# Performance work log

Measured on AMD Instinct MI355X. Metric: run time of the kernel, lower is better.

## Reference

```python
import jax, jax.numpy as jnp
import numpy as np

EPS = 1e-5  # torch BatchNorm1d default eps
NUM_CLASSES = 10


def setup_inputs() -> dict:
    key = jax.random.key(0)
    ks = jax.random.split(key, 8)
    N, M, D = 8192, 8192, 256
    h1, h2 = 128, 64
    x = jax.random.normal(ks[0], (N, D), dtype=jnp.float32)
    x_n = jax.random.normal(ks[1], (M, D), dtype=jnp.float32)
    y_n = jax.random.randint(ks[2], (M,), 0, NUM_CLASSES)
    # Linear weights (torch layout [out, in]) and biases
    W0 = jax.random.normal(ks[3], (h1, D), dtype=jnp.float32) * 0.05
    b0 = jnp.zeros((h1,), dtype=jnp.float32)
    W1 = jax.random.normal(ks[4], (h2, h1), dtype=jnp.float32) * 0.05
    b1 = jnp.zeros((h2,), dtype=jnp.float32)
    # BatchNorm1d affine params (torch init: weight=1, bias=0)
    g0 = jnp.ones((h1,), dtype=jnp.float32)
    bt0 = jnp.zeros((h1,), dtype=jnp.float32)
    g1 = jnp.ones((h2,), dtype=jnp.float32)
    bt1 = jnp.zeros((h2,), dtype=jnp.float32)
    return {"x": x, "x_n": x_n, "y_n": y_n,
            "W0": W0, "b0": b0, "g0": g0, "bt0": bt0,
            "W1": W1, "b1": b1, "g1": g1, "bt1": bt1}


def _bn(h, gamma, beta):
    # BatchNorm1d in training mode: batch mean / biased batch var per feature
    m = jnp.mean(h, axis=0)
    v = jnp.var(h, axis=0)
    return gamma * (h - m) / jnp.sqrt(v + EPS) + beta


def _feats(z, params):
    # fcn stack: BatchNorm(Tanh(Linear(z)))
    for W, b, g, bt in params:
        z = _bn(jnp.tanh(z @ W.T + b), g, bt)
    return z


def reference(x, x_n, y_n, W0, b0, g0, bt0, W1, b1, g1, bt1):
    params = [(W0, b0, g0, bt0), (W1, b1, g1, bt1)]
    q = _feats(x, params)    # [N, 64]
    k = _feats(x_n, params)  # [M, 64]
    # euclidean cdist via the quadratic expansion
    d2 = (jnp.sum(q * q, axis=1)[:, None]
          + jnp.sum(k * k, axis=1)[None, :]
          - 2.0 * (q @ k.T))
    sim = jnp.sqrt(jnp.maximum(d2, 1e-12))  # [N, M]
    sim = jnp.max(sim) - sim                 # larger = nearer
    # x != x_n here, so no self-mask branch (matches torch.equal check)
    p = jax.nn.softmax(sim, axis=1)          # [N, M]
    y1h = jax.nn.one_hot(y_n, NUM_CLASSES, dtype=p.dtype)  # [M, C]
    return jnp.clip(p @ y1h, 0.0, 1.0)       # [N, C]
```

## Files before the change

kernel.cpp:

```cpp
#include <hip/hip_runtime.h>
#include <math.h>

#define EPSBN 1e-5f
#define AADD(p, v) __hip_atomic_fetch_add((p), (v), __ATOMIC_RELAXED, __HIP_MEMORY_SCOPE_AGENT)

typedef unsigned short u16;
typedef short bf16x8 __attribute__((ext_vector_type(8)));
typedef float f32x4 __attribute__((ext_vector_type(4)));
typedef float f32x16 __attribute__((ext_vector_type(16)));
typedef int i32x4 __attribute__((ext_vector_type(4)));

constexpr int NROWS = 8192;
constexpr int NCLS = 10;
constexpr int MPAD = 8832;
constexpr int NT_PAD = 138;
constexpr int GY = 6;
constexpr int TPG = 23;
constexpr float SCL  = 2.0813689810056077f;
constexpr float SCL2 = -4.1627379620112154f;

constexpr size_t OFF_W0P = 0;
constexpr size_t OFF_H1H = 32768;
constexpr size_t OFF_H1L = OFF_H1H + 1048576;
constexpr size_t OFF_SUM = OFF_H1L + 1048576;
constexpr size_t OFF_W1P = OFF_SUM + 768;
constexpr size_t OFF_B1E = OFF_W1P + 16384;
constexpr size_t OFF_H2  = OFF_B1E + 128;
constexpr size_t OFF_PIDX = OFF_H2 + 1048576;
constexpr size_t OFF_TCLS = OFF_PIDX + MPAD;
constexpr size_t OFF_QH  = OFF_H1H;
constexpr size_t OFF_QL  = OFF_QH + 262144;
constexpr size_t OFF_QN2 = OFF_QL + 262144;
constexpr size_t OFF_KH  = OFF_QN2 + NROWS;
constexpr size_t OFF_KL  = OFF_KH + 282624;
constexpr size_t OFF_KN2 = OFF_KL + 282624;
constexpr size_t OFF_PART = OFF_H2;

__device__ inline u16 f2bf(float f) {
  unsigned u = __float_as_uint(f);
  unsigned r = (u + 0x7fffu + ((u >> 16) & 1u)) >> 16;
  return (u16)r;
}
__device__ inline float bf2f(u16 h) { return __uint_as_float(((unsigned)h) << 16); }

__device__ inline float tanh_fast(float x) {
  float e = __builtin_amdgcn_exp2f(x * 2.88539008f);
  return 1.f - 2.f * __builtin_amdgcn_rcpf(e + 1.f);
}

__global__ __launch_bounds__(256) void k_prep(
    const float* __restrict__ w0, const int* __restrict__ yn,
    u16* __restrict__ w0p, int* __restrict__ pidx, int* __restrict__ tcls,
    float* __restrict__ sums)
{
  if (blockIdx.x < 128) {
    int idx = blockIdx.x * 256 + threadIdx.x;
    int t = idx & 255;
    float v = w0[idx];
    u16 hi = f2bf(v);
    u16 lo = f2bf(v - bf2f(hi));
    int j = idx >> 8;
    w0p[(t >> 3) * 1024 + j * 8 + (t & 7)] = hi;
    w0p[32768 + (t >> 3) * 1024 + j * 8 + (t & 7)] = lo;
    return;
  }
  __shared__ int cnt[256][NCLS];
  __shared__ int wtot[4][NCLS];
  __shared__ int pstart[NCLS + 1];
  const int t = threadIdx.x;
  const int lane = t & 63, wv = t >> 6;
  sums[t] = 0.f; sums[t + 256] = 0.f; sums[t + 512] = 0.f;
  #pragma unroll
  for (int c = 0; c < NCLS; ++c) cnt[t][c] = 0;
  for (int i = t; i < MPAD; i += 256) pidx[i] = -1;
  for (int i = t; i < NROWS; i += 256) cnt[t][yn[i]]++;
  __syncthreads();
  #pragma unroll
  for (int c = 0; c < NCLS; ++c) {
    int x = cnt[t][c];
    int inc = x;
    #pragma unroll
    for (int d = 1; d < 64; d <<= 1) { int y = __shfl_up(inc, d); if (lane >= d) inc += y; }
    if (lane == 63) wtot[wv][c] = inc;
    cnt[t][c] = inc - x;
  }
  __syncthreads();
  if (t == 0) {
    int run = 0;
    #pragma unroll
    for (int c = 0; c < NCLS; ++c) {
      int tot = wtot[0][c] + wtot[1][c] + wtot[2][c] + wtot[3][c];
      pstart[c] = run;
      int ntile = (tot + 63) >> 6;
      for (int tt = 0; tt < ntile; ++tt) tcls[(run >> 6) + tt] = c;
      run += ntile << 6;
    }
    pstart[NCLS] = run;
    for (int tt = run >> 6; tt < NT_PAD; ++tt) tcls[tt] = NCLS;
  }
  __syncthreads();
  #pragma unroll
  for (int c = 0; c < NCLS; ++c) {
    int add = pstart[c];
    for (int w2 = 0; w2 < 4; ++w2) if (w2 < wv) add += wtot[w2][c];
    cnt[t][c] += add;
  }
  __syncthreads();
  for (int i = t; i < NROWS; i += 256) {
    int c = yn[i];
    pidx[cnt[t][c]++] = i;
  }
}

__global__ __launch_bounds__(256) void k_layer1(
    const float* __restrict__ x, const float* __restrict__ xn,
    const u16* __restrict__ w0p, const float* __restrict__ b0,
    u16* __restrict__ h1h, u16* __restrict__ h1l, float* __restrict__ sums)
{
  const int tid = threadIdx.x;
  const int w = tid >> 6, l = tid & 63;
  const int l15 = l & 15, l4 = l >> 4;
  const int blk = blockIdx.x;
  const int rowHalf = w & 1, colHalf = w >> 1;
  const int r0 = blk * 32 + 16 * rowHalf;
  const int c0 = 64 * colHalf;
  const int b = (blk < 256) ? 0 : 1;
  const float* src = (blk < 256) ? (x + (size_t)blk * 32 * 256)
                                 : (xn + (size_t)(blk - 256) * 32 * 256);
  const float* xrow = src + (size_t)(16 * rowHalf + l15) * 256;

  f32x4 acc[4];
  #pragma unroll
  for (int ct = 0; ct < 4; ++ct) acc[ct] = (f32x4){0.f, 0.f, 0.f, 0.f};

  #pragma unroll
  for (int ks = 0; ks < 8; ++ks) {
    const float* xp = xrow + ks * 32 + l4 * 8;
    f32x4 a0 = *(const f32x4*)xp;
    f32x4 a1 = *(const f32x4*)(xp + 4);
    bf16x8 ah, al_;
    #pragma unroll
    for (int i = 0; i < 4; ++i) {
      u16 h = f2bf(a0[i]); ah[i] = (short)h; al_[i] = (short)f2bf(a0[i] - bf2f(h));
    }
    #pragma unroll
    for (int i = 0; i < 4; ++i) {
      u16 h = f2bf(a1[i]); ah[4 + i] = (short)h; al_[4 + i] = (short)f2bf(a1[i] - bf2f(h));
    }
    const u16* bbase = w0p + (size_t)(ks * 4 + l4) * 1024;
    #pragma unroll
    for (int ct = 0; ct < 4; ++ct) {
      const int col = c0 + 16 * ct + l15;
      bf16x8 bh = *(const bf16x8*)(bbase + col * 8);
      bf16x8 bl = *(const bf16x8*)(bbase + 32768 + col * 8);
      acc[ct] = __builtin_amdgcn_mfma_f32_16x16x32_bf16(ah, bh, acc[ct], 0, 0, 0);
      acc[ct] = __builtin_amdgcn_mfma_f32_16x16x32_bf16(ah, bl, acc[ct], 0, 0, 0);
      acc[ct] = __builtin_amdgcn_mfma_f32_16x16x32_bf16(al_, bh, acc[ct], 0, 0, 0);
    }
  }

  #pragma unroll
  for (int ct = 0; ct < 4; ++ct) {
    const int col = c0 + 16 * ct + l15;
    const float bj = b0[col];
    float s = 0.f, q = 0.f;
    #pragma unroll
    for (int r = 0; r < 4; ++r) {
      float v = tanh_fast(acc[ct][r] + bj);
      const int row = r0 + 4 * l4 + r;
      u16 hi = f2bf(v);
      h1h[(size_t)row * 128 + col] = hi;
      h1l[(size_t)row * 128 + col] = f2bf(v - bf2f(hi));
      s += v; q += v * v;
    }
    s += __shfl_xor(s, 16); s += __shfl_xor(s, 32);
    q += __shfl_xor(q, 16); q += __shfl_xor(q, 32);
    if (l < 16) {
      AADD(&sums[b * 128 + col], s);
      AADD(&sums[256 + b * 128 + col], q);
    }
  }
}

__global__ __launch_bounds__(128) void k_foldp(
    const float* __restrict__ w1, const float* __restrict__ b1,
    const float* __restrict__ g0, const float* __restrict__ bt0,
    const float* __restrict__ sums, u16* __restrict__ w1p, float* __restrict__ b1e)
{
  const int o = blockIdx.x;
  const int j = threadIdx.x;
  __shared__ float red[2][2];
  const float w = w1[o * 128 + j];
  #pragma unroll
  for (int b = 0; b < 2; ++b) {
    float s = sums[b * 128 + j], q = sums[256 + b * 128 + j];
    float m = s * (1.f / 8192.f);
    float v = q * (1.f / 8192.f) - m * m;
    float sc = g0[j] * rsqrtf(v + EPSBN);
    float sh = bt0[j] - m * sc;
    float wsc = w * sc;
    u16 hi = f2bf(wsc);
    u16 lo = f2bf(wsc - bf2f(hi));
    w1p[((size_t)(b * 2 + 0) * 16 + (j >> 3)) * 512 + o * 8 + (j & 7)] = hi;
    w1p[((size_t)(b * 2 + 1) * 16 + (j >> 3)) * 512 + o * 8 + (j & 7)] = lo;
    float a = w * sh;
    #pragma unroll
    for (int off = 32; off; off >>= 1) a += __shfl_xor(a, off);
    if ((j & 63) == 0) red[j >> 6][b] = a;
  }
  __syncthreads();
  if (j < 2) b1e[j * 64 + o] = b1[o] + red[0][j] + red[1][j];
}

__global__ __launch_bounds__(256) void k_layer2(
    const u16* __restrict__ h1h, const u16* __restrict__ h1l,
    const u16* __restrict__ w1p, const float* __restrict__ b1e,
    float* __restrict__ h2, float* __restrict__ sums)
{
  const int tid = threadIdx.x;
  const int w = tid >> 6, l = tid & 63;
  const int l15 = l & 15, l4 = l >> 4;
  const int blk = blockIdx.x;
  const int rowHalf = w & 1, colHalf = w >> 1;
  const int r0 = blk * 32 + 16 * rowHalf;
  const int c0 = 32 * colHalf;
  const int b = blk >> 8;
  const u16* arow_h = h1h + (size_t)(r0 + l15) * 128;
  const u16* arow_l = h1l + (size_t)(r0 + l15) * 128;

  f32x4 acc[2];
  acc[0] = (f32x4){0.f, 0.f, 0.f, 0.f};
  acc[1] = (f32x4){0.f, 0.f, 0.f, 0.f};

  #pragma unroll
  for (int ks = 0; ks < 4; ++ks) {
    bf16x8 ah = *(const bf16x8*)(arow_h + ks * 32 + l4 * 8);
    bf16x8 al_ = *(const bf16x8*)(arow_l + ks * 32 + l4 * 8);
    const u16* bb = w1p + ((size_t)(b * 2) * 16 + ks * 4 + l4) * 512;
    #pragma unroll
    for (int ct = 0; ct < 2; ++ct) {
      const int col = c0 + 16 * ct + l15;
      bf16x8 bh = *(const bf16x8*)(bb + col * 8);
      bf16x8 bl = *(const bf16x8*)(bb + 8192 + col * 8);
      acc[ct] = __builtin_amdgcn_mfma_f32_16x16x32_bf16(ah, bh, acc[ct], 0, 0, 0);
      acc[ct] = __builtin_amdgcn_mfma_f32_16x16x32_bf16(ah, bl, acc[ct], 0, 0, 0);
      acc[ct] = __builtin_amdgcn_mfma_f32_16x16x32_bf16(al_, bh, acc[ct], 0, 0, 0);
    }
  }

  #pragma unroll
  for (int ct = 0; ct < 2; ++ct) {
    const int col = c0 + 16 * ct + l15;
    const float bj = b1e[b * 64 + col];
    float s = 0.f, q = 0.f;
    #pragma unroll
    for (int r = 0; r < 4; ++r) {
      float v = tanh_fast(acc[ct][r] + bj);
      const int row = r0 + 4 * l4 + r;
      h2[(size_t)row * 64 + col] = v;
      s += v; q += v * v;
    }
    s += __shfl_xor(s, 16); s += __shfl_xor(s, 32);
    q += __shfl_xor(q, 16); q += __shfl_xor(q, 32);
    if (l < 16) {
      AADD(&sums[512 + b * 64 + col], s);
      AADD(&sums[640 + b * 64 + col], q);
    }
  }
}

__global__ __launch_bounds__(256) void k_bn2(
    const float* __restrict__ h2, const float* __restrict__ sums,
    const float* __restrict__ g1, const float* __restrict__ bt1,
    const int* __restrict__ pidx,
    u16* __restrict__ qh, u16* __restrict__ ql, float* __restrict__ qn2,
    u16* __restrict__ kh, u16* __restrict__ kl, float* __restrict__ kn2)
{
  const int tid = threadIdx.x;
  const int r = tid >> 6, o = tid & 63;
  const bool isq = (blockIdx.x < 2048);
  const int b = isq ? 0 : 1;
  float s = sums[512 + b * 64 + o], q = sums[640 + b * 64 + o];
  float m = s * (1.f / 8192.f);
  float v = q * (1.f / 8192.f) - m * m;
  float sc = g1[o] * rsqrtf(v + EPSBN);
  float sh = bt1[o] - m * sc;
  if (isq) {
    const int row = blockIdx.x * 4 + r;
    float vv = sc * h2[(size_t)row * 64 + o] + sh;
    u16 hi = f2bf(vv);
    qh[(size_t)row * 64 + o] = hi;
    ql[(size_t)row * 64 + o] = f2bf(vv - bf2f(hi));
    float sq = vv * vv;
    #pragma unroll
    for (int off = 32; off; off >>= 1) sq += __shfl_xor(sq, off);
    if (o == 0) qn2[row] = SCL * sq;
  } else {
    const int row = (blockIdx.x - 2048) * 4 + r;
    const int src = pidx[row];
    float vv = 0.f;
    if (src >= 0) vv = sc * h2[(size_t)(NROWS + src) * 64 + o] + sh;
    u16 hi = f2bf(vv);
    kh[(size_t)row * 64 + o] = hi;
    kl[(size_t)row * 64 + o] = f2bf(vv - bf2f(hi));
    float sq = vv * vv;
    #pragma unroll
    for (int off = 32; off; off >>= 1) sq += __shfl_xor(sq, off);
    if (o == 0) kn2[row] = (src >= 0) ? SCL * sq : 1e30f;
  }
}

__global__ __launch_bounds__(256, 3) void k_dist(
    const u16* __restrict__ qh, const u16* __restrict__ ql, const float* __restrict__ qn2,
    const u16* __restrict__ kh, const u16* __restrict__ kl, const float* __restrict__ kn2,
    const int* __restrict__ tcls, float* __restrict__ part)
{
  __shared__ u16 bs[2][8192];
  __shared__ float cls_lds[2 * (NCLS + 1) * 64];
  const int tid = threadIdx.x;
  const int w = tid >> 6, l = tid & 63;
  const int n0 = blockIdx.x * 64;
  const int g = blockIdx.y;
  const int t0 = g * TPG, t1 = t0 + TPG;

  for (int i = tid; i < 2 * (NCLS + 1) * 64; i += 256) cls_lds[i] = 0.f;

  const int lh = l >> 5;
  const int arow = n0 + 32 * (w >> 1) + (l & 31);
  bf16x8 aH[4], aL[4];
  #pragma unroll
  for (int j = 0; j < 4; ++j) {
    aH[j] = *(const bf16x8*)(qh + (size_t)arow * 64 + j * 16 + 8 * lh);
    aL[j] = *(const bf16x8*)(ql + (size_t)arow * 64 + j * 16 + 8 * lh);
  }
  float qnr[16];
  #pragma unroll
  for (int g4 = 0; g4 < 4; ++g4) {
    f32x4 qv = *(const f32x4*)(qn2 + n0 + 32 * (w >> 1) + 8 * g4 + 4 * lh);
    qnr[4 * g4 + 0] = qv[0]; qnr[4 * g4 + 1] = qv[1];
    qnr[4 * g4 + 2] = qv[2]; qnr[4 * g4 + 3] = qv[3];
  }

  const int sarr = w & 1, shalf = w >> 1;
  const u16* sbase = (sarr ? kl : kh) + (size_t)l * 64 + shalf * 32;
  const int c7l = l & 7;
  char* wb_base = (char*)&bs[0][0] + l * 256 + sarr * 128;
  const int ws0 = (((shalf * 4 + 0) ^ c7l) << 4);
  const int ws1 = (((shalf * 4 + 1) ^ c7l) << 4);
  const int ws2 = (((shalf * 4 + 2) ^ c7l) << 4);
  const int ws3 = (((shalf * 4 + 3) ^ c7l) << 4);

  const int colL = 32 * (w & 1) + (l & 31);
  const char* rb_base = (const char*)&bs[0][0] + colL * 256;
  const int c7r = colL & 7;

  i32x4 st0, st1, st2, st3;
#define LOADST(TT) do { const u16* sp_ = sbase + (size_t)(TT) * 4096; \
    st0 = *(const i32x4*)(sp_);      st1 = *(const i32x4*)(sp_ + 8);  \
    st2 = *(const i32x4*)(sp_ + 16); st3 = *(const i32x4*)(sp_ + 24); } while (0)
#define WRITEST(PB) do { char* d_ = wb_base + (PB) * 16384; \
    *(i32x4*)(d_ + ws0) = st0; *(i32x4*)(d_ + ws1) = st1; \
    *(i32x4*)(d_ + ws2) = st2; *(i32x4*)(d_ + ws3) = st3; } while (0)
#define FLUSH(CC) do { \
    _Pragma("unroll") for (int r = 0; r < 16; ++r) { \
      run[r] += __shfl_xor(run[r], 1);  run[r] += __shfl_xor(run[r], 2); \
      run[r] += __shfl_xor(run[r], 4);  run[r] += __shfl_xor(run[r], 8); \
      run[r] += __shfl_xor(run[r], 16); } \
    if ((l & 31) == 0) { \
      float* cl_ = cls_lds + (w & 1) * 704 + (CC) * 64 + 32 * (w >> 1) + 4 * lh; \
      _Pragma("unroll") for (int r = 0; r < 16; ++r) cl_[(r & 3) + 8 * (r >> 2)] += run[r]; } \
    _Pragma("unroll") for (int r = 0; r < 16; ++r) run[r] = 0.f; } while (0)

  LOADST(t0);
  WRITEST(0);
  LOADST(t0 + 1);

  float run[16];
  #pragma unroll
  for (int r = 0; r < 16; ++r) run[r] = 0.f;
  int ccur = tcls[t0];
  int p = 0;

  for (int t = t0; t < t1; ++t) {
    __syncthreads();
    if (t + 1 < t1) WRITEST(p ^ 1);
    if (t + 2 < t1) LOADST(t + 2);
    const int c = tcls[t];
    if (c != ccur) { FLUSH(ccur); ccur = c; }
    const float kv = kn2[t * 64 + colL];

    f32x16 acc;
    #pragma unroll
    for (int r = 0; r < 16; ++r) acc[r] = 0.f;
    const char* pb = rb_base + p * 16384;
    #pragma unroll
    for (int j = 0; j < 4; ++j) {
      const int c8 = 2 * j + lh;
      bf16x8 bh  = *(const bf16x8*)(pb + ((c8 ^ c7r) << 4));
      bf16x8 bl_ = *(const bf16x8*)(pb + 128 + ((c8 ^ c7r) << 4));
      acc = __builtin_amdgcn_mfma_f32_32x32x16_bf16(aH[j], bh,  acc, 0, 0, 0);
      acc = __builtin_amdgcn_mfma_f32_32x32x16_bf16(aH[j], bl_, acc, 0, 0, 0);
      acc = __builtin_amdgcn_mfma_f32_32x32x16_bf16(aL[j], bh,  acc, 0, 0, 0);
    }
    #pragma unroll
    for (int r = 0; r < 16; ++r) {
      float d2 = fmaf(SCL2, acc[r], qnr[r] + kv);
      d2 = fmaxf(d2, 2.0813689e-12f);
      run[r] += __builtin_amdgcn_exp2f(-__builtin_amdgcn_sqrtf(d2));
    }
    p ^= 1;
  }
  FLUSH(ccur);
  __syncthreads();

  for (int i = tid; i < (NCLS + 1) * 64; i += 256) {
    const int c = i >> 6, rr = i & 63;
    part[((size_t)g * (NCLS + 1) + c) * NROWS + n0 + rr] = cls_lds[i] + cls_lds[704 + i];
  }
#undef LOADST
#undef WRITEST
#undef FLUSH
}

__global__ __launch_bounds__(256) void k_final(const float* __restrict__ part,
                                               float* __restrict__ out)
{
  const int n = blockIdx.x * 256 + threadIdx.x;
  float sc[NCLS];
  #pragma unroll
  for (int c = 0; c < NCLS; ++c) sc[c] = 0.f;
  for (int g = 0; g < GY; ++g) {
    #pragma unroll
    for (int c = 0; c < NCLS; ++c)
      sc[c] += part[((size_t)g * (NCLS + 1) + c) * NROWS + n];
  }
  float tot = 0.f;
  #pragma unroll
  for (int c = 0; c < NCLS; ++c) tot += sc[c];
  const float inv = 1.f / tot;
  #pragma unroll
  for (int c = 0; c < NCLS; ++c)
    out[(size_t)n * NCLS + c] = fminf(fmaxf(sc[c] * inv, 0.f), 1.f);
}

extern "C" void kernel_launch(void* const* d_in, const int* in_sizes, int n_in,
                              void* d_out, int out_size, void* d_ws, size_t ws_size,
                              hipStream_t stream) {
  const float* x   = (const float*)d_in[0];
  const float* xn  = (const float*)d_in[1];
  const int*   yn  = (const int*)d_in[2];
  const float* W0  = (const float*)d_in[3];
  const float* b0  = (const float*)d_in[4];
  const float* g0  = (const float*)d_in[5];
  const float* bt0 = (const float*)d_in[6];
  const float* W1  = (const float*)d_in[7];
  const float* b1  = (const float*)d_in[8];
  const float* g1  = (const float*)d_in[9];
  const float* bt1 = (const float*)d_in[10];
  float* out = (float*)d_out;
  float* ws  = (float*)d_ws;

  u16*   w0pp = (u16*)(ws + OFF_W0P);
  u16*   h1hp = (u16*)(ws + OFF_H1H);
  u16*   h1lp = (u16*)(ws + OFF_H1L);
  float* sumsp= ws + OFF_SUM;
  u16*   w1pp = (u16*)(ws + OFF_W1P);
  float* b1ep = ws + OFF_B1E;
  float* h2p  = ws + OFF_H2;
  int*   pidxp= (int*)(ws + OFF_PIDX);
  int*   tclsp= (int*)(ws + OFF_TCLS);
  u16*   qhp  = (u16*)(ws + OFF_QH);
  u16*   qlp  = (u16*)(ws + OFF_QL);
  float* qn2p = ws + OFF_QN2;
  u16*   khp  = (u16*)(ws + OFF_KH);
  u16*   klp  = (u16*)(ws + OFF_KL);
  float* kn2p = ws + OFF_KN2;
  float* partp= ws + OFF_PART;

  k_prep<<<129, 256, 0, stream>>>(W0, yn, w0pp, pidxp, tclsp, sumsp);
  k_layer1<<<512, 256, 0, stream>>>(x, xn, w0pp, b0, h1hp, h1lp, sumsp);
  k_foldp<<<64, 128, 0, stream>>>(W1, b1, g0, bt0, sumsp, w1pp, b1ep);
  k_layer2<<<512, 256, 0, stream>>>(h1hp, h1lp, w1pp, b1ep, h2p, sumsp);
  k_bn2<<<2048 + MPAD / 4, 256, 0, stream>>>(h2p, sumsp, g1, bt1, pidxp,
                                             qhp, qlp, qn2p, khp, klp, kn2p);
  k_dist<<<dim3(128, GY), 256, 0, stream>>>(qhp, qlp, qn2p, khp, klp, kn2p, tclsp, partp);
  k_final<<<32, 256, 0, stream>>>(partp, out);
}
```

Before: 137.4 us.

## Stage key tiles via direct global-to-LDS loads and split MFMA accumulators

Replaces the register-staged key tile copy (global load to VGPRs, then an LDS write) with global_load_lds direct transfers, keeping the XOR swizzle by computing per-lane source offsets. The dependent MFMA chain is split into two accumulators to shorten the latency chain. The column-tile split grows from 6 to 8 groups with uneven ranges, and the occupancy hint rises from 3 to 4 blocks per CU. These changes aim to cut register pressure and VALU/LDS write overhead, at the cost of more partial outputs for the final reduction and possible register spills under the tighter launch bound.

Result: slower. 152.7 us (+11.1%).

```diff
diff --git a/kernel.cpp b/kernel.cpp
--- a/kernel.cpp
+++ b/kernel.cpp
@@ -14,8 +14,7 @@
 constexpr int NCLS = 10;
 constexpr int MPAD = 8832;
 constexpr int NT_PAD = 138;
-constexpr int GY = 6;
-constexpr int TPG = 23;
+constexpr int GY = 8;
 constexpr float SCL  = 2.0813689810056077f;
 constexpr float SCL2 = -4.1627379620112154f;
 
@@ -48,6 +47,12 @@
   return 1.f - 2.f * __builtin_amdgcn_rcpf(e + 1.f);
 }
 
+__device__ inline void glds16(const u16* g, u16* l) {
+  __builtin_amdgcn_global_load_lds(
+      (const __attribute__((address_space(1))) unsigned int*)g,
+      (__attribute__((address_space(3))) unsigned int*)l, 16, 0, 0);
+}
+
 __global__ __launch_bounds__(256) void k_prep(
     const float* __restrict__ w0, const int* __restrict__ yn,
     u16* __restrict__ w0p, int* __restrict__ pidx, int* __restrict__ tcls,
@@ -310,7 +315,7 @@
   }
 }
 
-__global__ __launch_bounds__(256, 3) void k_dist(
+__global__ __launch_bounds__(256, 4) void k_dist(
     const u16* __restrict__ qh, const u16* __restrict__ ql, const float* __restrict__ qn2,
     const u16* __restrict__ kh, const u16* __restrict__ kl, const float* __restrict__ kn2,
     const int* __restrict__ tcls, float* __restrict__ part)
@@ -321,7 +326,7 @@
   const int w = tid >> 6, l = tid & 63;
   const int n0 = blockIdx.x * 64;
   const int g = blockIdx.y;
-  const int t0 = g * TPG, t1 = t0 + TPG;
+  const int t0 = (g * NT_PAD) / GY, t1 = ((g + 1) * NT_PAD) / GY;
 
   for (int i = tid; i < 2 * (NCLS + 1) * 64; i += 256) cls_lds[i] = 0.f;
 
@@ -341,26 +346,27 @@
     qnr[4 * g4 + 2] = qv[2]; qnr[4 * g4 + 3] = qv[3];
   }
 
-  const int sarr = w & 1, shalf = w >> 1;
-  const u16* sbase = (sarr ? kl : kh) + (size_t)l * 64 + shalf * 32;
-  const int c7l = l & 7;
-  char* wb_base = (char*)&bs[0][0] + l * 256 + sarr * 128;
-  const int ws0 = (((shalf * 4 + 0) ^ c7l) << 4);
-  const int ws1 = (((shalf * 4 + 1) ^ c7l) << 4);
-  const int ws2 = (((shalf * 4 + 2) ^ c7l) << 4);
-  const int ws3 = (((shalf * 4 + 3) ^ c7l) << 4);
+  const int a_ = (l >> 3) & 1;
+  const u16* sarr = a_ ? kl : kh;
+  int soff[4];
+  #pragma unroll
+  for (int j = 0; j < 4; ++j) {
+    const int col = 16 * w + 4 * j + (l >> 4);
+    const int c8 = (l & 7) ^ (col & 7);
+    soff[j] = col * 64 + c8 * 8;
+  }
 
   const int colL = 32 * (w & 1) + (l & 31);
   const char* rb_base = (const char*)&bs[0][0] + colL * 256;
   const int c7r = colL & 7;
 
-  i32x4 st0, st1, st2, st3;
-#define LOADST(TT) do { const u16* sp_ = sbase + (size_t)(TT) * 4096; \
-    st0 = *(const i32x4*)(sp_);      st1 = *(const i32x4*)(sp_ + 8);  \
-    st2 = *(const i32x4*)(sp_ + 16); st3 = *(const i32x4*)(sp_ + 24); } while (0)
-#define WRITEST(PB) do { char* d_ = wb_base + (PB) * 16384; \
-    *(i32x4*)(d_ + ws0) = st0; *(i32x4*)(d_ + ws1) = st1; \
-    *(i32x4*)(d_ + ws2) = st2; *(i32x4*)(d_ + ws3) = st3; } while (0)
+#define STAGE(TT, PB) do { const size_t tb_ = (size_t)(TT) * 4096; \
+    u16* lb_ = &bs[PB][0] + (size_t)(w * 4) * 512; \
+    glds16(sarr + tb_ + soff[0], lb_);        \
+    glds16(sarr + tb_ + soff[1], lb_ + 512);  \
+    glds16(sarr + tb_ + soff[2], lb_ + 1024); \
+    glds16(sarr + tb_ + soff[3], lb_ + 1536); } while (0)
+
 #define FLUSH(CC) do { \
     _Pragma("unroll") for (int r = 0; r < 16; ++r) { \
       run[r] += __shfl_xor(run[r], 1);  run[r] += __shfl_xor(run[r], 2); \
@@ -371,9 +377,7 @@
       _Pragma("unroll") for (int r = 0; r < 16; ++r) cl_[(r & 3) + 8 * (r >> 2)] += run[r]; } \
     _Pragma("unroll") for (int r = 0; r < 16; ++r) run[r] = 0.f; } while (0)
 
-  LOADST(t0);
-  WRITEST(0);
-  LOADST(t0 + 1);
+  STAGE(t0, 0);
 
   float run[16];
   #pragma unroll
@@ -383,28 +387,27 @@
 
   for (int t = t0; t < t1; ++t) {
     __syncthreads();
-    if (t + 1 < t1) WRITEST(p ^ 1);
-    if (t + 2 < t1) LOADST(t + 2);
+    if (t + 1 < t1) STAGE(t + 1, p ^ 1);
     const int c = tcls[t];
     if (c != ccur) { FLUSH(ccur); ccur = c; }
     const float kv = kn2[t * 64 + colL];
 
-    f32x16 acc;
-    #pragma unroll
-    for (int r = 0; r < 16; ++r) acc[r] = 0.f;
+    f32x16 accA, accB;
+    #pragma unroll
+    for (int r = 0; r < 16; ++r) { accA[r] = 0.f; accB[r] = 0.f; }
     const char* pb = rb_base + p * 16384;
     #pragma unroll
     for (int j = 0; j < 4; ++j) {
       const int c8 = 2 * j + lh;
       bf16x8 bh  = *(const bf16x8*)(pb + ((c8 ^ c7r) << 4));
       bf16x8 bl_ = *(const bf16x8*)(pb + 128 + ((c8 ^ c7r) << 4));
-      acc = __builtin_amdgcn_mfma_f32_32x32x16_bf16(aH[j], bh,  acc, 0, 0, 0);
-      acc = __builtin_amdgcn_mfma_f32_32x32x16_bf16(aH[j], bl_, acc, 0, 0, 0);
-      acc = __builtin_amdgcn_mfma_f32_32x32x16_bf16(aL[j], bh,  acc, 0, 0, 0);
+      accA = __builtin_amdgcn_mfma_f32_32x32x16_bf16(aH[j], bh,  accA, 0, 0, 0);
+      accB = __builtin_amdgcn_mfma_f32_32x32x16_bf16(aH[j], bl_, accB, 0, 0, 0);
+      accA = __builtin_amdgcn_mfma_f32_32x32x16_bf16(aL[j], bh,  accA, 0, 0, 0);
     }
     #pragma unroll
     for (int r = 0; r < 16; ++r) {
-      float d2 = fmaf(SCL2, acc[r], qnr[r] + kv);
+      float d2 = fmaf(SCL2, accA[r] + accB[r], qnr[r] + kv);
       d2 = fmaxf(d2, 2.0813689e-12f);
       run[r] += __builtin_amdgcn_exp2f(-__builtin_amdgcn_sqrtf(d2));
     }
@@ -417,8 +420,7 @@
     const int c = i >> 6, rr = i & 63;
     part[((size_t)g * (NCLS + 1) + c) * NROWS + n0 + rr] = cls_lds[i] + cls_lds[704 + i];
   }
-#undef LOADST
-#undef WRITEST
+#undef STAGE
 #undef FLUSH
 }
 
```
